# Optimization experiments

Measured on AMD Instinct MI355X. Metric: run time of the kernel, lower is better.

Reference implementation:

```python
import jax, jax.numpy as jnp
import numpy as np

NEG_BIG = -9.0e15

def setup_inputs() -> dict:
    key = jax.random.key(0)
    k1, k2, k3, k4 = jax.random.split(key, 4)
    N, F_in, F_out = 2048, 512, 64
    x = jax.random.normal(k1, (N, F_in), dtype=jnp.float32)
    adj = jax.random.randint(k2, (N, N), 0, 2, dtype=jnp.int32)
    # xavier_uniform with gain=1.414
    def xavier(k, shape, gain=1.414):
        fan_in, fan_out = shape[0], shape[1]
        bound = gain * np.sqrt(6.0 / (fan_in + fan_out))
        return jax.random.uniform(k, shape, jnp.float32, -bound, bound)
    W = xavier(k3, (F_in, F_out))
    a = xavier(k4, (F_out, 1))
    return {"x": x, "adj": adj, "W": W, "a": a}

def reference(x, adj, W, a):
    h = x @ W                                  # [N, F_out]
    # pairwise |h_i - h_j| projected by a: e[i,j] = relu(sum_f |h_i,f - h_j,f| * a_f)
    diff = jnp.abs(h[:, None, :] - h[None, :, :])   # [N, N, F_out]
    e = jax.nn.relu(jnp.einsum('ijf,fo->ij', diff, a))  # [N, N]
    scores = jnp.where(adj > 0, e, NEG_BIG)
    attention = jax.nn.softmax(scores, axis=1)
    out = attention @ h                        # [N, F_out]
    return jax.nn.relu(out)                    # concat=True path
```

## Files before the change

kernel.cpp:

```cpp
#include <hip/hip_runtime.h>

#define Nn 2048
#define FIN 512
#define FO 64
#define SHIFT 20.0f
#define NJT 16
#define JR (Nn / NJT)
#define LS 66
#define PTS 68

__global__ __launch_bounds__(256) void gat_zero(float* __restrict__ z) {
    z[blockIdx.x * 256 + threadIdx.x] = 0.f;
}

__global__ __launch_bounds__(256) void gat_xw(const float* __restrict__ x,
                                              const float* __restrict__ W,
                                              float* __restrict__ h) {
    __shared__ float part[2][2][FO];
    const int wave = threadIdx.x >> 6;
    const int lane = threadIdx.x & 63;
    const int rs = wave >> 1;
    const int kh = wave & 1;
    int row = blockIdx.x * 2 + rs;
    row = __builtin_amdgcn_readfirstlane(row);
    const float* xr = x + (size_t)row * FIN + kh * (FIN / 2);
    const float* Wp = W + (size_t)kh * (FIN / 2) * FO;
    float acc = 0.f;
#pragma unroll 2
    for (int k = 0; k < FIN / 2; k += 8) {
        float4 xa = *(const float4*)(xr + k);
        float4 xb = *(const float4*)(xr + k + 4);
        acc = fmaf(xa.x, Wp[(k + 0) * FO + lane], acc);
        acc = fmaf(xa.y, Wp[(k + 1) * FO + lane], acc);
        acc = fmaf(xa.z, Wp[(k + 2) * FO + lane], acc);
        acc = fmaf(xa.w, Wp[(k + 3) * FO + lane], acc);
        acc = fmaf(xb.x, Wp[(k + 4) * FO + lane], acc);
        acc = fmaf(xb.y, Wp[(k + 5) * FO + lane], acc);
        acc = fmaf(xb.z, Wp[(k + 6) * FO + lane], acc);
        acc = fmaf(xb.w, Wp[(k + 7) * FO + lane], acc);
    }
    part[rs][kh][lane] = acc;
    __syncthreads();
    if (threadIdx.x < 128) {
        const int r2 = threadIdx.x >> 6;
        const int l2 = threadIdx.x & 63;
        h[((size_t)blockIdx.x * 2 + r2) * FO + l2] = part[r2][0][l2] + part[r2][1][l2];
    }
}

__global__ __launch_bounds__(256) void gat_attn3(const float* __restrict__ h,
                                                 const int* __restrict__ adj,
                                                 const float* __restrict__ a,
                                                 float* __restrict__ osum,
                                                 float* __restrict__ lsum) {
    __shared__ float hi_s[64 * LS];
    __shared__ float hj_s[64 * LS];
    __shared__ float pT_s[64 * PTS];
    __shared__ float a_s[FO];

    const int tid = threadIdx.x;
    const int w = tid >> 6;
    const int lane = tid & 63;
    const int li = lane & 3;
    const int lj = lane >> 2;
    const int it = blockIdx.x >> 4;
    const int jt = blockIdx.x & (NJT - 1);
    const int ib = it * 64;
    const int jb = jt * JR;
    const int iw = w * 16;

    for (int g4 = tid; g4 < 1024; g4 += 256) {
        float4 v = *(const float4*)(h + (size_t)ib * FO + (size_t)g4 * 4);
        float* d = &hi_s[(g4 >> 4) * LS + (g4 & 15) * 4];
        *(float2*)d = make_float2(v.x, v.y);
        *(float2*)(d + 2) = make_float2(v.z, v.w);
    }
    if (tid < FO) a_s[tid] = a[tid];

    float pv[4][4];
    float ls[4];
#pragma unroll
    for (int u = 0; u < 4; u++) {
        ls[u] = 0.f;
#pragma unroll
        for (int v2 = 0; v2 < 4; v2++) pv[u][v2] = 0.f;
    }

    for (int jc = 0; jc < JR; jc += 64) {
        __syncthreads();
        const float* hsrc = h + (size_t)(jb + jc) * FO;
        for (int g4 = tid; g4 < 1024; g4 += 256) {
            float4 v = *(const float4*)(hsrc + (size_t)g4 * 4);
            float* d = &hj_s[(g4 >> 4) * LS + (g4 & 15) * 4];
            *(float2*)d = make_float2(v.x, v.y);
            *(float2*)(d + 2) = make_float2(v.z, v.w);
        }
        __syncthreads();

        int4 am[4];
#pragma unroll
        for (int di = 0; di < 4; di++)
            am[di] = *(const int4*)(adj + (size_t)(ib + iw + 4 * li + di) * Nn + (jb + jc + 4 * lj));

        float e[4][4];
#pragma unroll
        for (int di = 0; di < 4; di++)
#pragma unroll
            for (int dj = 0; dj < 4; dj++) e[di][dj] = 0.f;

#pragma unroll 4
        for (int f = 0; f < FO; f += 2) {
            const float2 av = *(const float2*)&a_s[f];
            float2 hi[4], hj[4];
#pragma unroll
            for (int d = 0; d < 4; d++) {
                hi[d] = *(const float2*)&hi_s[(iw + 4 * li + d) * LS + f];
                hj[d] = *(const float2*)&hj_s[(4 * lj + d) * LS + f];
            }
#pragma unroll
            for (int di = 0; di < 4; di++)
#pragma unroll
                for (int dj = 0; dj < 4; dj++) {
                    e[di][dj] = fmaf(fabsf(hi[di].x - hj[dj].x), av.x, e[di][dj]);
                    e[di][dj] = fmaf(fabsf(hi[di].y - hj[dj].y), av.y, e[di][dj]);
                }
        }

#pragma unroll
        for (int di = 0; di < 4; di++) {
            const int* ap = (const int*)&am[di];
#pragma unroll
            for (int dj = 0; dj < 4; dj++) {
                const float p = (ap[dj] > 0) ? __expf(fmaxf(e[di][dj], 0.f) - SHIFT) : 0.f;
                e[di][dj] = p;
                ls[di] += p;
            }
        }

#pragma unroll
        for (int dj = 0; dj < 4; dj++) {
            *(float4*)&pT_s[(4 * lj + dj) * PTS + iw + 4 * li] =
                make_float4(e[0][dj], e[1][dj], e[2][dj], e[3][dj]);
        }
        __syncthreads();

#pragma unroll 4
        for (int j = 0; j < 64; j++) {
            const float4 pj = *(const float4*)&pT_s[j * PTS + iw + 4 * li];
            const float2 h0 = *(const float2*)&hj_s[j * LS + 4 * lj];
            const float2 h1 = *(const float2*)&hj_s[j * LS + 4 * lj + 2];
            pv[0][0] = fmaf(pj.x, h0.x, pv[0][0]);
            pv[0][1] = fmaf(pj.x, h0.y, pv[0][1]);
            pv[0][2] = fmaf(pj.x, h1.x, pv[0][2]);
            pv[0][3] = fmaf(pj.x, h1.y, pv[0][3]);
            pv[1][0] = fmaf(pj.y, h0.x, pv[1][0]);
            pv[1][1] = fmaf(pj.y, h0.y, pv[1][1]);
            pv[1][2] = fmaf(pj.y, h1.x, pv[1][2]);
            pv[1][3] = fmaf(pj.y, h1.y, pv[1][3]);
            pv[2][0] = fmaf(pj.z, h0.x, pv[2][0]);
            pv[2][1] = fmaf(pj.z, h0.y, pv[2][1]);
            pv[2][2] = fmaf(pj.z, h1.x, pv[2][2]);
            pv[2][3] = fmaf(pj.z, h1.y, pv[2][3]);
            pv[3][0] = fmaf(pj.w, h0.x, pv[3][0]);
            pv[3][1] = fmaf(pj.w, h0.y, pv[3][1]);
            pv[3][2] = fmaf(pj.w, h1.x, pv[3][2]);
            pv[3][3] = fmaf(pj.w, h1.y, pv[3][3]);
        }
    }

#pragma unroll
    for (int di = 0; di < 4; di++) {
        float v = ls[di];
        v += __shfl_xor(v, 4, 64);
        v += __shfl_xor(v, 8, 64);
        v += __shfl_xor(v, 16, 64);
        v += __shfl_xor(v, 32, 64);
        ls[di] = v;
    }
    if (lj == 0) {
#pragma unroll
        for (int di = 0; di < 4; di++)
            atomicAdd(&lsum[ib + iw + 4 * li + di], ls[di]);
    }
#pragma unroll
    for (int di = 0; di < 4; di++) {
#pragma unroll
        for (int v2 = 0; v2 < 4; v2++)
            atomicAdd(&osum[(size_t)(ib + iw + 4 * li + di) * FO + 4 * lj + v2], pv[di][v2]);
    }
}

__global__ __launch_bounds__(256) void gat_fin(const float* __restrict__ osum,
                                               const float* __restrict__ lsum,
                                               float* __restrict__ out) {
    const int t = blockIdx.x * 256 + threadIdx.x;
    out[t] = fmaxf(osum[t] / lsum[t >> 6], 0.f);
}

extern "C" void kernel_launch(void* const* d_in, const int* in_sizes, int n_in,
                              void* d_out, int out_size, void* d_ws, size_t ws_size,
                              hipStream_t stream) {
    const float* x   = (const float*)d_in[0];
    const int*   adj = (const int*)d_in[1];
    const float* W   = (const float*)d_in[2];
    const float* a   = (const float*)d_in[3];
    float* out = (float*)d_out;

    float* h    = (float*)d_ws;
    float* osum = h + (size_t)Nn * FO;
    float* lsum = osum + (size_t)Nn * FO;

    gat_zero<<<dim3(520), dim3(256), 0, stream>>>(osum);
    gat_xw<<<dim3(1024), dim3(256), 0, stream>>>(x, W, h);
    gat_attn3<<<dim3(32 * NJT), dim3(256), 0, stream>>>(h, adj, a, osum, lsum);
    gat_fin<<<dim3(512), dim3(256), 0, stream>>>(osum, lsum, out);
}
```

Before: 136.3 us.

## Split attention over more j-tiles, alias shared buffers, fold zeroing into xw

Doubles the number of j-tiles so each attention block handles a single 64-column chunk, which removes the inner chunk loop and doubles the grid to 1024 blocks. hi_s and pT_s now share one shared-memory buffer, and a launch-bounds occupancy hint of 4 is added to raise residency. The separate zeroing kernel is merged into gat_xw, saving one launch. In exchange, each block does one tile of work with fixed setup overhead, and twice as many atomicAdds go to osum and lsum.

```diff
diff --git a/kernel.cpp b/kernel.cpp
--- a/kernel.cpp
+++ b/kernel.cpp
@@ -4,18 +4,19 @@
 #define FIN 512
 #define FO 64
 #define SHIFT 20.0f
-#define NJT 16
+#define NJT 32
 #define JR (Nn / NJT)
 #define LS 66
 #define PTS 68
-
-__global__ __launch_bounds__(256) void gat_zero(float* __restrict__ z) {
-    z[blockIdx.x * 256 + threadIdx.x] = 0.f;
-}
+#define ZTOT (Nn * FO + Nn)
 
 __global__ __launch_bounds__(256) void gat_xw(const float* __restrict__ x,
                                               const float* __restrict__ W,
-                                              float* __restrict__ h) {
+                                              float* __restrict__ h,
+                                              float* __restrict__ z) {
+    const int gt = blockIdx.x * 256 + threadIdx.x;
+    if (gt < ZTOT) z[gt] = 0.f;
+
     __shared__ float part[2][2][FO];
     const int wave = threadIdx.x >> 6;
     const int lane = threadIdx.x & 63;
@@ -48,22 +49,23 @@
     }
 }
 
-__global__ __launch_bounds__(256) void gat_attn3(const float* __restrict__ h,
-                                                 const int* __restrict__ adj,
-                                                 const float* __restrict__ a,
-                                                 float* __restrict__ osum,
-                                                 float* __restrict__ lsum) {
-    __shared__ float hi_s[64 * LS];
+__global__ __launch_bounds__(256, 4) void gat_attn3(const float* __restrict__ h,
+                                                    const int* __restrict__ adj,
+                                                    const float* __restrict__ a,
+                                                    float* __restrict__ osum,
+                                                    float* __restrict__ lsum) {
+    __shared__ float up[64 * PTS];
     __shared__ float hj_s[64 * LS];
-    __shared__ float pT_s[64 * PTS];
     __shared__ float a_s[FO];
+    float* hi_s = up;
+    float* pT_s = up;
 
     const int tid = threadIdx.x;
     const int w = tid >> 6;
     const int lane = tid & 63;
     const int li = lane & 3;
     const int lj = lane >> 2;
-    const int it = blockIdx.x >> 4;
+    const int it = blockIdx.x >> 5;
     const int jt = blockIdx.x & (NJT - 1);
     const int ib = it * 64;
     const int jb = jt * JR;
@@ -74,8 +76,18 @@
         float* d = &hi_s[(g4 >> 4) * LS + (g4 & 15) * 4];
         *(float2*)d = make_float2(v.x, v.y);
         *(float2*)(d + 2) = make_float2(v.z, v.w);
+        float4 u = *(const float4*)(h + (size_t)jb * FO + (size_t)g4 * 4);
+        float* e2 = &hj_s[(g4 >> 4) * LS + (g4 & 15) * 4];
+        *(float2*)e2 = make_float2(u.x, u.y);
+        *(float2*)(e2 + 2) = make_float2(u.z, u.w);
     }
     if (tid < FO) a_s[tid] = a[tid];
+    __syncthreads();
+
+    int4 am[4];
+#pragma unroll
+    for (int di = 0; di < 4; di++)
+        am[di] = *(const int4*)(adj + (size_t)(ib + iw + 4 * li + di) * Nn + (jb + 4 * lj));
 
     float pv[4][4];
     float ls[4];
@@ -86,86 +98,71 @@
         for (int v2 = 0; v2 < 4; v2++) pv[u][v2] = 0.f;
     }
 
-    for (int jc = 0; jc < JR; jc += 64) {
-        __syncthreads();
-        const float* hsrc = h + (size_t)(jb + jc) * FO;
-        for (int g4 = tid; g4 < 1024; g4 += 256) {
-            float4 v = *(const float4*)(hsrc + (size_t)g4 * 4);
-            float* d = &hj_s[(g4 >> 4) * LS + (g4 & 15) * 4];
-            *(float2*)d = make_float2(v.x, v.y);
-            *(float2*)(d + 2) = make_float2(v.z, v.w);
+    float e[4][4];
+#pragma unroll
+    for (int di = 0; di < 4; di++)
+#pragma unroll
+        for (int dj = 0; dj < 4; dj++) e[di][dj] = 0.f;
+
+#pragma unroll 4
+    for (int f = 0; f < FO; f += 2) {
+        const float2 av = *(const float2*)&a_s[f];
+        float2 hi[4], hj[4];
+#pragma unroll
+        for (int d = 0; d < 4; d++) {
+            hi[d] = *(const float2*)&hi_s[(iw + 4 * li + d) * LS + f];
+            hj[d] = *(const float2*)&hj_s[(4 * lj + d) * LS + f];
         }
-        __syncthreads();
-
-        int4 am[4];
 #pragma unroll
         for (int di = 0; di < 4; di++)
-            am[di] = *(const int4*)(adj + (size_t)(ib + iw + 4 * li + di) * Nn + (jb + jc + 4 * lj));
-
-        float e[4][4];
-#pragma unroll
-        for (int di = 0; di < 4; di++)
-#pragma unroll
-            for (int dj = 0; dj < 4; dj++) e[di][dj] = 0.f;
+#pragma unroll
+            for (int dj = 0; dj < 4; dj++) {
+                e[di][dj] = fmaf(fabsf(hi[di].x - hj[dj].x), av.x, e[di][dj]);
+                e[di][dj] = fmaf(fabsf(hi[di].y - hj[dj].y), av.y, e[di][dj]);
+            }
+    }
+
+#pragma unroll
+    for (int di = 0; di < 4; di++) {
+        const int* ap = (const int*)&am[di];
+#pragma unroll
+        for (int dj = 0; dj < 4; dj++) {
+            const float p = (ap[dj] > 0) ? __expf(fmaxf(e[di][dj], 0.f) - SHIFT) : 0.f;
+            e[di][dj] = p;
+            ls[di] += p;
+        }
+    }
+
+    __syncthreads();
+
+#pragma unroll
+    for (int dj = 0; dj < 4; dj++) {
+        *(float4*)&pT_s[(4 * lj + dj) * PTS + iw + 4 * li] =
+            make_float4(e[0][dj], e[1][dj], e[2][dj], e[3][dj]);
+    }
+    __syncthreads();
 
 #pragma unroll 4
-        for (int f = 0; f < FO; f += 2) {
-            const float2 av = *(const float2*)&a_s[f];
-            float2 hi[4], hj[4];
-#pragma unroll
-            for (int d = 0; d < 4; d++) {
-                hi[d] = *(const float2*)&hi_s[(iw + 4 * li + d) * LS + f];
-                hj[d] = *(const float2*)&hj_s[(4 * lj + d) * LS + f];
-            }
-#pragma unroll
-            for (int di = 0; di < 4; di++)
-#pragma unroll
-                for (int dj = 0; dj < 4; dj++) {
-                    e[di][dj] = fmaf(fabsf(hi[di].x - hj[dj].x), av.x, e[di][dj]);
-                    e[di][dj] = fmaf(fabsf(hi[di].y - hj[dj].y), av.y, e[di][dj]);
-                }
-        }
-
-#pragma unroll
-        for (int di = 0; di < 4; di++) {
-            const int* ap = (const int*)&am[di];
-#pragma unroll
-            for (int dj = 0; dj < 4; dj++) {
-                const float p = (ap[dj] > 0) ? __expf(fmaxf(e[di][dj], 0.f) - SHIFT) : 0.f;
-                e[di][dj] = p;
-                ls[di] += p;
-            }
-        }
-
-#pragma unroll
-        for (int dj = 0; dj < 4; dj++) {
-            *(float4*)&pT_s[(4 * lj + dj) * PTS + iw + 4 * li] =
-                make_float4(e[0][dj], e[1][dj], e[2][dj], e[3][dj]);
-        }
-        __syncthreads();
-
-#pragma unroll 4
-        for (int j = 0; j < 64; j++) {
-            const float4 pj = *(const float4*)&pT_s[j * PTS + iw + 4 * li];
-            const float2 h0 = *(const float2*)&hj_s[j * LS + 4 * lj];
-            const float2 h1 = *(const float2*)&hj_s[j * LS + 4 * lj + 2];
-            pv[0][0] = fmaf(pj.x, h0.x, pv[0][0]);
-            pv[0][1] = fmaf(pj.x, h0.y, pv[0][1]);
-            pv[0][2] = fmaf(pj.x, h1.x, pv[0][2]);
-            pv[0][3] = fmaf(pj.x, h1.y, pv[0][3]);
-            pv[1][0] = fmaf(pj.y, h0.x, pv[1][0]);
-            pv[1][1] = fmaf(pj.y, h0.y, pv[1][1]);
-            pv[1][2] = fmaf(pj.y, h1.x, pv[1][2]);
-            pv[1][3] = fmaf(pj.y, h1.y, pv[1][3]);
-            pv[2][0] = fmaf(pj.z, h0.x, pv[2][0]);
-            pv[2][1] = fmaf(pj.z, h0.y, pv[2][1]);
-            pv[2][2] = fmaf(pj.z, h1.x, pv[2][2]);
-            pv[2][3] = fmaf(pj.z, h1.y, pv[2][3]);
-            pv[3][0] = fmaf(pj.w, h0.x, pv[3][0]);
-            pv[3][1] = fmaf(pj.w, h0.y, pv[3][1]);
-            pv[3][2] = fmaf(pj.w, h1.x, pv[3][2]);
-            pv[3][3] = fmaf(pj.w, h1.y, pv[3][3]);
-        }
+    for (int j = 0; j < 64; j++) {
+        const float4 pj = *(const float4*)&pT_s[j * PTS + iw + 4 * li];
+        const float2 h0 = *(const float2*)&hj_s[j * LS + 4 * lj];
+        const float2 h1 = *(const float2*)&hj_s[j * LS + 4 * lj + 2];
+        pv[0][0] = fmaf(pj.x, h0.x, pv[0][0]);
+        pv[0][1] = fmaf(pj.x, h0.y, pv[0][1]);
+        pv[0][2] = fmaf(pj.x, h1.x, pv[0][2]);
+        pv[0][3] = fmaf(pj.x, h1.y, pv[0][3]);
+        pv[1][0] = fmaf(pj.y, h0.x, pv[1][0]);
+        pv[1][1] = fmaf(pj.y, h0.y, pv[1][1]);
+        pv[1][2] = fmaf(pj.y, h1.x, pv[1][2]);
+        pv[1][3] = fmaf(pj.y, h1.y, pv[1][3]);
+        pv[2][0] = fmaf(pj.z, h0.x, pv[2][0]);
+        pv[2][1] = fmaf(pj.z, h0.y, pv[2][1]);
+        pv[2][2] = fmaf(pj.z, h1.x, pv[2][2]);
+        pv[2][3] = fmaf(pj.z, h1.y, pv[2][3]);
+        pv[3][0] = fmaf(pj.w, h0.x, pv[3][0]);
+        pv[3][1] = fmaf(pj.w, h0.y, pv[3][1]);
+        pv[3][2] = fmaf(pj.w, h1.x, pv[3][2]);
+        pv[3][3] = fmaf(pj.w, h1.y, pv[3][3]);
     }
 
 #pragma unroll
@@ -210,8 +207,7 @@
     float* osum = h + (size_t)Nn * FO;
     float* lsum = osum + (size_t)Nn * FO;
 
-    gat_zero<<<dim3(520), dim3(256), 0, stream>>>(osum);
-    gat_xw<<<dim3(1024), dim3(256), 0, stream>>>(x, W, h);
+    gat_xw<<<dim3(1024), dim3(256), 0, stream>>>(x, W, h, osum);
     gat_attn3<<<dim3(32 * NJT), dim3(256), 0, stream>>>(h, adj, a, osum, lsum);
     gat_fin<<<dim3(512), dim3(256), 0, stream>>>(osum, lsum, out);
 }
```

Measured after the change: 151.9 us. +11.4%, slower.
